# Kernel tuning notes

Measured on AMD Instinct MI355X. Metric: run time of the kernel, lower is better.

The kernel has to match this reference:

```python
import jax, jax.numpy as jnp
import numpy as np

N_NODES = 50000
N_EDGES = 800000
IN_FEATS = 128
OUT_FEATS = 16
NUM_HEADS = 8
NEG_SLOPE = 0.2


def setup_inputs() -> dict:
    key = jax.random.key(0)
    k1, k2, k3, k4, k5 = jax.random.split(key, 5)
    feat = jax.random.normal(k1, (N_NODES, IN_FEATS), dtype=jnp.float32)
    src = jax.random.randint(k2, (N_EDGES,), 0, N_NODES, dtype=jnp.int32)
    dst = jax.random.randint(k3, (N_EDGES,), 0, N_NODES, dtype=jnp.int32)
    # fc weight stored as [in, H*Dout] so y = x @ W (equivalent to torch Linear)
    W = jax.random.normal(k4, (IN_FEATS, NUM_HEADS * OUT_FEATS), dtype=jnp.float32) * 0.05
    attn_weights = jax.random.normal(k5, (2 * NUM_HEADS * OUT_FEATS,), dtype=jnp.float32) * 0.1
    bias = jnp.zeros((NUM_HEADS * OUT_FEATS,), dtype=jnp.float32)
    return {"feat": feat, "W": W, "attn_weights": attn_weights, "bias": bias,
            "src": src, "dst": dst}


def reference(feat, W, attn_weights, bias, src, dst):
    H, D = NUM_HEADS, OUT_FEATS
    N = feat.shape[0]
    # Linear projection: [N, H, D]
    h = (feat @ W).reshape(N, H, D)
    a = attn_weights.reshape(2, H, D)
    # per-node attention logits per head
    e_src = jnp.einsum("nhd,hd->nh", h, a[0])  # source side
    e_dst = jnp.einsum("nhd,hd->nh", h, a[1])  # destination side
    # per-edge scores: [E, H]
    e = e_src[src] + e_dst[dst]
    e = jnp.where(e > 0, e, NEG_SLOPE * e)  # LeakyReLU
    # segment softmax over incoming edges of each dst node
    m = jax.ops.segment_max(e, dst, num_segments=N)          # [N, H]
    m = jnp.where(jnp.isfinite(m), m, 0.0)
    ex = jnp.exp(e - m[dst])                                  # [E, H]
    denom = jax.ops.segment_sum(ex, dst, num_segments=N)     # [N, H]
    alpha = ex / jnp.where(denom[dst] > 0, denom[dst], 1.0)  # [E, H]
    # weighted aggregation of source features: [N, H, D]
    out = jax.ops.segment_sum(alpha[:, :, None] * h[src], dst, num_segments=N)
    out = out + bias.reshape(1, H, D)
    return out
```

## Files before the change

### kernel.cpp

```cpp
#include <hip/hip_runtime.h>
#include <hip/hip_bf16.h>

#define H_HEADS 8
#define D_OUT 16
#define C_FEATS 128
#define NEG_SLOPE 0.2f

typedef __attribute__((ext_vector_type(8))) short short8;
typedef __attribute__((ext_vector_type(4))) float f32x4;

__device__ inline unsigned short f2bf(float f) {
    __hip_bfloat16 b = __float2bfloat16(f);
    return *reinterpret_cast<unsigned short*>(&b);
}
__device__ inline float bf2f(unsigned short u) {
    return __uint_as_float((unsigned)u << 16);
}
__device__ inline float bf_lo(unsigned u) { return __uint_as_float(u << 16); }
__device__ inline float bf_hi(unsigned u) { return __uint_as_float(u & 0xffff0000u); }

__global__ __launch_bounds__(256) void k_prep(const float* __restrict__ W,
                                              unsigned short* __restrict__ Wfh,
                                              unsigned short* __restrict__ Wfl,
                                              int* __restrict__ deg, int N) {
    const int b = blockIdx.x, t = threadIdx.x;
    if (b < 8) {
        const int idx = b * 256 + t;
        const int frag = idx >> 6, lane = idx & 63;
        const int kc = frag >> 3, nt = frag & 7;
        const int kb = kc * 32 + ((lane >> 4) << 3);
        const int col = nt * 16 + (lane & 15);
        unsigned short hs[8], ls[8];
#pragma unroll
        for (int i = 0; i < 8; ++i) {
            const float x = W[(size_t)(kb + i) * C_FEATS + col];
            const unsigned short hh = f2bf(x);
            hs[i] = hh;
            ls[i] = f2bf(x - bf2f(hh));
        }
        uint4 uh, ul;
        uh.x = hs[0] | ((unsigned)hs[1] << 16);
        uh.y = hs[2] | ((unsigned)hs[3] << 16);
        uh.z = hs[4] | ((unsigned)hs[5] << 16);
        uh.w = hs[6] | ((unsigned)hs[7] << 16);
        ul.x = ls[0] | ((unsigned)ls[1] << 16);
        ul.y = ls[2] | ((unsigned)ls[3] << 16);
        ul.z = ls[4] | ((unsigned)ls[5] << 16);
        ul.w = ls[6] | ((unsigned)ls[7] << 16);
        *reinterpret_cast<uint4*>(&Wfh[(size_t)idx * 8]) = uh;
        *reinterpret_cast<uint4*>(&Wfl[(size_t)idx * 8]) = ul;
    } else {
        const int i = (b - 8) * 256 + t;
        if (i < N) deg[i] = 0;
    }
}

__global__ __launch_bounds__(512) void k_gemm_deg(
    const float* __restrict__ feat, const unsigned short* __restrict__ Wfh,
    const unsigned short* __restrict__ Wfl, const int* __restrict__ dst,
    int* __restrict__ deg, int* __restrict__ rank, unsigned short* __restrict__ h16,
    int N, int E, int degBlocks) {
    const int t = threadIdx.x;
    if ((int)blockIdx.x < degBlocks) {
        const int stride = degBlocks * 512;
        for (int e = blockIdx.x * 512 + t; e < E; e += stride)
            rank[e] = atomicAdd(&deg[dst[e]], 1);
        return;
    }
    __shared__ uint4 sW[4096];
    {
        const uint4* gh = reinterpret_cast<const uint4*>(Wfh);
        const uint4* gl = reinterpret_cast<const uint4*>(Wfl);
#pragma unroll
        for (int i = 0; i < 4; ++i) {
            const int j = t + i * 512;
            sW[j] = gh[j];
            sW[j + 2048] = gl[j];
        }
    }
    __syncthreads();

    const int bid = blockIdx.x - degBlocks;
    const int w = t >> 6, lane = t & 63;
    const int rbase = bid * 128 + w * 16;
    const int rowA = rbase + (lane & 15);
    const int ko = (lane >> 4) << 3;
    const bool rv = rowA < N;
    const float* fr = feat + (size_t)rowA * C_FEATS;

    f32x4 acc[8];
#pragma unroll
    for (int nt = 0; nt < 8; ++nt)
#pragma unroll
        for (int j = 0; j < 4; ++j) acc[nt][j] = 0.f;

#pragma unroll
    for (int kc = 0; kc < 4; ++kc) {
        float4 x0 = make_float4(0.f, 0.f, 0.f, 0.f), x1 = x0;
        if (rv) {
            x0 = *reinterpret_cast<const float4*>(fr + kc * 32 + ko);
            x1 = *reinterpret_cast<const float4*>(fr + kc * 32 + ko + 4);
        }
        const float xs[8] = {x0.x, x0.y, x0.z, x0.w, x1.x, x1.y, x1.z, x1.w};
        short8 ah, al;
#pragma unroll
        for (int i = 0; i < 8; ++i) {
            const unsigned short hh = f2bf(xs[i]);
            ah[i] = (short)hh;
            al[i] = (short)f2bf(xs[i] - bf2f(hh));
        }
#pragma unroll
        for (int nt = 0; nt < 8; ++nt) {
            const int fi = (kc * 8 + nt) * 64 + lane;
            const short8 bh = *reinterpret_cast<const short8*>(&sW[fi]);
            const short8 bl = *reinterpret_cast<const short8*>(&sW[fi + 2048]);
            acc[nt] = __builtin_amdgcn_mfma_f32_16x16x32_bf16(ah, bh, acc[nt], 0, 0, 0);
            acc[nt] = __builtin_amdgcn_mfma_f32_16x16x32_bf16(al, bh, acc[nt], 0, 0, 0);
            acc[nt] = __builtin_amdgcn_mfma_f32_16x16x32_bf16(ah, bl, acc[nt], 0, 0, 0);
        }
    }
    const int r0 = rbase + ((lane >> 4) << 2);
    const int colc = lane & 15;
#pragma unroll
    for (int nt = 0; nt < 8; ++nt) {
#pragma unroll
        for (int r = 0; r < 4; ++r) {
            const int row = r0 + r;
            if (row < N)
                h16[(size_t)row * C_FEATS + nt * 16 + colc] = f2bf(acc[nt][r]);
        }
    }
}

__global__ __launch_bounds__(256) void k_logits_bsum(
    const unsigned short* __restrict__ h16, const float* __restrict__ aw,
    float* __restrict__ es, float* __restrict__ ed,
    const int* __restrict__ deg, int* __restrict__ bsum, int N, int LB) {
    const int t = threadIdx.x;
    if ((int)blockIdx.x < LB) {
        const int idx = blockIdx.x * 256 + t;
        if (idx >= N * H_HEADS) return;
        const int n = idx >> 3, hh = idx & 7;
        const uint4 u0 = *reinterpret_cast<const uint4*>(&h16[(size_t)n * C_FEATS + hh * 16]);
        const uint4 u1 = *reinterpret_cast<const uint4*>(&h16[(size_t)n * C_FEATS + hh * 16 + 8]);
        float hv[16];
        hv[0] = bf_lo(u0.x);  hv[1] = bf_hi(u0.x);
        hv[2] = bf_lo(u0.y);  hv[3] = bf_hi(u0.y);
        hv[4] = bf_lo(u0.z);  hv[5] = bf_hi(u0.z);
        hv[6] = bf_lo(u0.w);  hv[7] = bf_hi(u0.w);
        hv[8] = bf_lo(u1.x);  hv[9] = bf_hi(u1.x);
        hv[10] = bf_lo(u1.y); hv[11] = bf_hi(u1.y);
        hv[12] = bf_lo(u1.z); hv[13] = bf_hi(u1.z);
        hv[14] = bf_lo(u1.w); hv[15] = bf_hi(u1.w);
        float s0 = 0.f, s1 = 0.f;
#pragma unroll
        for (int j = 0; j < 16; ++j) {
            s0 = fmaf(hv[j], aw[hh * 16 + j], s0);
            s1 = fmaf(hv[j], aw[C_FEATS + hh * 16 + j], s1);
        }
        es[idx] = s0;
        ed[idx] = s1;
    } else {
        const int i = (blockIdx.x - LB) * 256 + t;
        int v = (i < N) ? deg[i] : 0;
#pragma unroll
        for (int m = 1; m < 64; m <<= 1) v += __shfl_xor(v, m, 64);
        __shared__ int ws[4];
        if ((t & 63) == 0) ws[t >> 6] = v;
        __syncthreads();
        if (t == 0) bsum[blockIdx.x - LB] = ws[0] + ws[1] + ws[2] + ws[3];
    }
}

__device__ inline int block_scan_incl(int v) {
    int lane = threadIdx.x & 63, w = threadIdx.x >> 6;
    int x = v;
#pragma unroll
    for (int d = 1; d < 64; d <<= 1) {
        int u = __shfl_up(x, d, 64);
        if (lane >= d) x += u;
    }
    __shared__ int wsum[4];
    if (lane == 63) wsum[w] = x;
    __syncthreads();
    int add = 0;
    for (int k = 0; k < w; ++k) add += wsum[k];
    return x + add;
}

__global__ void k_scanb(const int* __restrict__ bsum, int* __restrict__ bpre,
                        int NB, int* __restrict__ offs, int N) {
    int t = threadIdx.x;
    int v = (t < NB) ? bsum[t] : 0;
    int incl = block_scan_incl(v);
    if (t < NB) bpre[t] = incl - v;
    if (t == NB - 1) offs[N] = incl;
}

__global__ void k_scanc(const int* __restrict__ deg, const int* __restrict__ bpre,
                        int* __restrict__ offs, int N) {
    int i = blockIdx.x * 256 + threadIdx.x;
    int v = (i < N) ? deg[i] : 0;
    int incl = block_scan_incl(v);
    int excl = incl - v + bpre[blockIdx.x];
    if (i < N) offs[i] = excl;
}

__global__ void k_scatter(const int* __restrict__ src, const int* __restrict__ dst,
                          const int* __restrict__ rank, const int* __restrict__ offs,
                          int* __restrict__ ssorted, int E) {
    int e = blockIdx.x * 256 + threadIdx.x;
    if (e < E)
        ssorted[offs[dst[e]] + rank[e]] = src[e];
}

__global__ __launch_bounds__(256) void k_agg(const unsigned short* __restrict__ h16,
                                             const float* __restrict__ es,
                                             const float* __restrict__ ed,
                                             const int* __restrict__ offs,
                                             const int* __restrict__ ssorted,
                                             const float* __restrict__ bias,
                                             float* __restrict__ out, int N) {
    const int wid = threadIdx.x >> 6, lane = threadIdx.x & 63;
    const int n = blockIdx.x * 4 + wid;
    if (n >= N) return;
    const int beg = offs[n];
    const int deg = offs[n + 1] - beg;

    const int hh = lane >> 3, j0 = lane & 7;
    const float edv = ed[(size_t)n * H_HEADS + hh];

    const int cl = lane & 15, q = lane >> 4;
    const int ah = cl >> 1;
    const int ab = ah << 3;
    float acc[8];
#pragma unroll
    for (int k = 0; k < 8; ++k) acc[k] = 0.f;

    float m = -1e30f, s = 0.f;

    if (deg <= 32) {
        int snc[4];
        float evc[4];
#pragma unroll
        for (int c = 0; c < 4; ++c) {
            const int j = c * 8 + j0;
            const bool va = (j < deg);
            int sn = 0;
            float ev = -1e30f;
            if (va) {
                sn = ssorted[beg + j];
                float t = es[(size_t)sn * H_HEADS + hh] + edv;
                ev = t > 0.f ? t : NEG_SLOPE * t;
                if (ev > m) {
                    s = s * __expf(m - ev) + 1.f;
                    m = ev;
                } else {
                    s += __expf(ev - m);
                }
            }
            snc[c] = sn;
            evc[c] = ev;
        }
#pragma unroll
        for (int msk = 1; msk < 8; msk <<= 1) {
            float mo = __shfl_xor(m, msk, 64);
            float so = __shfl_xor(s, msk, 64);
            float mn = fmaxf(m, mo);
            s = s * __expf(m - mn) + so * __expf(mo - mn);
            m = mn;
        }
        const float inv = (s > 0.f) ? 1.f / s : 0.f;

#pragma unroll
        for (int c = 0; c < 4; ++c) {
            const int cb = c * 8;
            if (cb >= deg) break;
            const float alpha = (cb + j0 < deg) ? __expf(evc[c] - m) * inv : 0.f;
            const int sn = snc[c];
            int rem = deg - cb; if (rem > 8) rem = 8;
#pragma unroll
            for (int e4 = 0; e4 < 2; ++e4) {
                if (4 * e4 >= rem) break;
                const int s0 = __shfl(sn, 4 * e4 + 0, 64);
                const int s1 = __shfl(sn, 4 * e4 + 1, 64);
                const int s2 = __shfl(sn, 4 * e4 + 2, 64);
                const int s3 = __shfl(sn, 4 * e4 + 3, 64);
                const int snq = (q == 0) ? s0 : (q == 1) ? s1 : (q == 2) ? s2 : s3;
                const float al = __shfl(alpha, ab + 4 * e4 + q, 64);
                const uint4 hv = *reinterpret_cast<const uint4*>(
                    &h16[(size_t)snq * C_FEATS + cl * 8]);
                acc[0] = fmaf(al, bf_lo(hv.x), acc[0]);
                acc[1] = fmaf(al, bf_hi(hv.x), acc[1]);
                acc[2] = fmaf(al, bf_lo(hv.y), acc[2]);
                acc[3] = fmaf(al, bf_hi(hv.y), acc[3]);
                acc[4] = fmaf(al, bf_lo(hv.z), acc[4]);
                acc[5] = fmaf(al, bf_hi(hv.z), acc[5]);
                acc[6] = fmaf(al, bf_lo(hv.w), acc[6]);
                acc[7] = fmaf(al, bf_hi(hv.w), acc[7]);
            }
        }
    } else {
        for (int e = j0; e < deg; e += 8) {
            int sn = ssorted[beg + e];
            float ev = es[(size_t)sn * H_HEADS + hh] + edv;
            ev = ev > 0.f ? ev : NEG_SLOPE * ev;
            if (ev > m) {
                s = s * __expf(m - ev) + 1.f;
                m = ev;
            } else {
                s += __expf(ev - m);
            }
        }
#pragma unroll
        for (int msk = 1; msk < 8; msk <<= 1) {
            float mo = __shfl_xor(m, msk, 64);
            float so = __shfl_xor(s, msk, 64);
            float mn = fmaxf(m, mo);
            s = s * __expf(m - mn) + so * __expf(mo - mn);
            m = mn;
        }
        const float inv = (s > 0.f) ? 1.f / s : 0.f;

        for (int cb = 0; cb < deg; cb += 8) {
            const int j = cb + j0;
            int sn = 0;
            float alpha = 0.f;
            if (j < deg) {
                sn = ssorted[beg + j];
                float t = es[(size_t)sn * H_HEADS + hh] + edv;
                t = t > 0.f ? t : NEG_SLOPE * t;
                alpha = __expf(t - m) * inv;
            }
            int rem = deg - cb; if (rem > 8) rem = 8;
#pragma unroll
            for (int e4 = 0; e4 < 2; ++e4) {
                if (4 * e4 >= rem) break;
                const int s0 = __shfl(sn, 4 * e4 + 0, 64);
                const int s1 = __shfl(sn, 4 * e4 + 1, 64);
                const int s2 = __shfl(sn, 4 * e4 + 2, 64);
                const int s3 = __shfl(sn, 4 * e4 + 3, 64);
                const int snq = (q == 0) ? s0 : (q == 1) ? s1 : (q == 2) ? s2 : s3;
                const float al = __shfl(alpha, ab + 4 * e4 + q, 64);
                const uint4 hv = *reinterpret_cast<const uint4*>(
                    &h16[(size_t)snq * C_FEATS + cl * 8]);
                acc[0] = fmaf(al, bf_lo(hv.x), acc[0]);
                acc[1] = fmaf(al, bf_hi(hv.x), acc[1]);
                acc[2] = fmaf(al, bf_lo(hv.y), acc[2]);
                acc[3] = fmaf(al, bf_hi(hv.y), acc[3]);
                acc[4] = fmaf(al, bf_lo(hv.z), acc[4]);
                acc[5] = fmaf(al, bf_hi(hv.z), acc[5]);
                acc[6] = fmaf(al, bf_lo(hv.w), acc[6]);
                acc[7] = fmaf(al, bf_hi(hv.w), acc[7]);
            }
        }
    }

#pragma unroll
    for (int k = 0; k < 8; ++k) {
        acc[k] += __shfl_xor(acc[k], 16, 64);
        acc[k] += __shfl_xor(acc[k], 32, 64);
    }
    if (q == 0) {
        const float4 b0 = *reinterpret_cast<const float4*>(&bias[cl * 8]);
        const float4 b1 = *reinterpret_cast<const float4*>(&bias[cl * 8 + 4]);
        float4 o0 = make_float4(acc[0] + b0.x, acc[1] + b0.y, acc[2] + b0.z, acc[3] + b0.w);
        float4 o1 = make_float4(acc[4] + b1.x, acc[5] + b1.y, acc[6] + b1.z, acc[7] + b1.w);
        *reinterpret_cast<float4*>(&out[(size_t)n * C_FEATS + cl * 8]) = o0;
        *reinterpret_cast<float4*>(&out[(size_t)n * C_FEATS + cl * 8 + 4]) = o1;
    }
}

extern "C" void kernel_launch(void* const* d_in, const int* in_sizes, int n_in,
                              void* d_out, int out_size, void* d_ws, size_t ws_size,
                              hipStream_t stream) {
    const float* feat = (const float*)d_in[0];
    const float* W    = (const float*)d_in[1];
    const float* aw   = (const float*)d_in[2];
    const float* bias = (const float*)d_in[3];
    const int*   src  = (const int*)d_in[4];
    const int*   dst  = (const int*)d_in[5];
    float* out = (float*)d_out;

    const int N = in_sizes[0] / C_FEATS;
    const int E = in_sizes[4];
    const int NB = (N + 255) / 256;
    const int GB = (N + 127) / 128;
    const int DB = 256;
    const int LB = (N * H_HEADS + 255) / 256;

    char* p = (char*)d_ws;
    auto take = [&](size_t bytes) {
        char* q = p;
        p += (bytes + 255) & ~size_t(255);
        return q;
    };
    unsigned short* h16 = (unsigned short*)take((size_t)N * C_FEATS * 2);
    float* es      = (float*)take((size_t)N * H_HEADS * 4);
    float* edt     = (float*)take((size_t)N * H_HEADS * 4);
    int*   deg     = (int*)take((size_t)N * 4);
    int*   offs    = (int*)take((size_t)(N + 1) * 4);
    int*   bsum    = (int*)take((size_t)NB * 4);
    int*   bpre    = (int*)take((size_t)NB * 4);
    int*   ssorted = (int*)take((size_t)E * 4);
    int*   rank    = (int*)take((size_t)E * 4);
    unsigned short* Wfh = (unsigned short*)take((size_t)C_FEATS * C_FEATS * 2);
    unsigned short* Wfl = (unsigned short*)take((size_t)C_FEATS * C_FEATS * 2);
    (void)ws_size;

    k_prep<<<8 + NB, 256, 0, stream>>>(W, Wfh, Wfl, deg, N);
    k_gemm_deg<<<DB + GB, 512, 0, stream>>>(feat, Wfh, Wfl, dst, deg, rank, h16, N, E, DB);
    k_logits_bsum<<<LB + NB, 256, 0, stream>>>(h16, aw, es, edt, deg, bsum, N, LB);
    k_scanb<<<1, 256, 0, stream>>>(bsum, bpre, NB, offs, N);
    k_scanc<<<NB, 256, 0, stream>>>(deg, bpre, offs, N);
    k_scatter<<<(E + 255) / 256, 256, 0, stream>>>(src, dst, rank, offs, ssorted, E);
    k_agg<<<(N + 3) / 4, 256, 0, stream>>>(h16, es, edt, offs, ssorted, bias, out, N);
}
```

Baseline: 119.6 us.

## Fuse attention logits into GEMM epilogue and split degree counting kernel

```diff
diff --git a/kernel.cpp b/kernel.cpp
--- a/kernel.cpp
+++ b/kernel.cpp
@@ -55,18 +55,20 @@
     }
 }
 
-__global__ __launch_bounds__(512) void k_gemm_deg(
+__global__ __launch_bounds__(256) void k_deg_rank(const int* __restrict__ dst,
+                                                  int* __restrict__ deg,
+                                                  int* __restrict__ rank, int E) {
+    const int e = blockIdx.x * 256 + threadIdx.x;
+    if (e < E)
+        rank[e] = atomicAdd(&deg[dst[e]], 1);
+}
+
+__global__ __launch_bounds__(512) void k_gemm(
     const float* __restrict__ feat, const unsigned short* __restrict__ Wfh,
-    const unsigned short* __restrict__ Wfl, const int* __restrict__ dst,
-    int* __restrict__ deg, int* __restrict__ rank, unsigned short* __restrict__ h16,
-    int N, int E, int degBlocks) {
+    const unsigned short* __restrict__ Wfl, const float* __restrict__ aw,
+    unsigned short* __restrict__ h16, float* __restrict__ es,
+    float* __restrict__ ed, int N) {
     const int t = threadIdx.x;
-    if ((int)blockIdx.x < degBlocks) {
-        const int stride = degBlocks * 512;
-        for (int e = blockIdx.x * 512 + t; e < E; e += stride)
-            rank[e] = atomicAdd(&deg[dst[e]], 1);
-        return;
-    }
     __shared__ uint4 sW[4096];
     {
         const uint4* gh = reinterpret_cast<const uint4*>(Wfh);
@@ -80,7 +82,7 @@
     }
     __syncthreads();
 
-    const int bid = blockIdx.x - degBlocks;
+    const int bid = blockIdx.x;
     const int w = t >> 6, lane = t & 63;
     const int rbase = bid * 128 + w * 16;
     const int rowA = rbase + (lane & 15);
@@ -130,46 +132,37 @@
                 h16[(size_t)row * C_FEATS + nt * 16 + colc] = f2bf(acc[nt][r]);
         }
     }
-}
-
-__global__ __launch_bounds__(256) void k_logits_bsum(
-    const unsigned short* __restrict__ h16, const float* __restrict__ aw,
-    float* __restrict__ es, float* __restrict__ ed,
-    const int* __restrict__ deg, int* __restrict__ bsum, int N, int LB) {
-    const int t = threadIdx.x;
-    if ((int)blockIdx.x < LB) {
-        const int idx = blockIdx.x * 256 + t;
-        if (idx >= N * H_HEADS) return;
-        const int n = idx >> 3, hh = idx & 7;
-        const uint4 u0 = *reinterpret_cast<const uint4*>(&h16[(size_t)n * C_FEATS + hh * 16]);
-        const uint4 u1 = *reinterpret_cast<const uint4*>(&h16[(size_t)n * C_FEATS + hh * 16 + 8]);
-        float hv[16];
-        hv[0] = bf_lo(u0.x);  hv[1] = bf_hi(u0.x);
-        hv[2] = bf_lo(u0.y);  hv[3] = bf_hi(u0.y);
-        hv[4] = bf_lo(u0.z);  hv[5] = bf_hi(u0.z);
-        hv[6] = bf_lo(u0.w);  hv[7] = bf_hi(u0.w);
-        hv[8] = bf_lo(u1.x);  hv[9] = bf_hi(u1.x);
-        hv[10] = bf_lo(u1.y); hv[11] = bf_hi(u1.y);
-        hv[12] = bf_lo(u1.z); hv[13] = bf_hi(u1.z);
-        hv[14] = bf_lo(u1.w); hv[15] = bf_hi(u1.w);
-        float s0 = 0.f, s1 = 0.f;
-#pragma unroll
-        for (int j = 0; j < 16; ++j) {
-            s0 = fmaf(hv[j], aw[hh * 16 + j], s0);
-            s1 = fmaf(hv[j], aw[C_FEATS + hh * 16 + j], s1);
-        }
-        es[idx] = s0;
-        ed[idx] = s1;
-    } else {
-        const int i = (blockIdx.x - LB) * 256 + t;
-        int v = (i < N) ? deg[i] : 0;
-#pragma unroll
-        for (int m = 1; m < 64; m <<= 1) v += __shfl_xor(v, m, 64);
-        __shared__ int ws[4];
-        if ((t & 63) == 0) ws[t >> 6] = v;
-        __syncthreads();
-        if (t == 0) bsum[blockIdx.x - LB] = ws[0] + ws[1] + ws[2] + ws[3];
-    }
+#pragma unroll
+    for (int nt = 0; nt < 8; ++nt) {
+        const float wa = aw[nt * 16 + colc];
+        const float wb = aw[C_FEATS + nt * 16 + colc];
+#pragma unroll
+        for (int r = 0; r < 4; ++r) {
+            float pe = acc[nt][r] * wa;
+            float pd = acc[nt][r] * wb;
+#pragma unroll
+            for (int msk = 1; msk <= 8; msk <<= 1) {
+                pe += __shfl_xor(pe, msk, 64);
+                pd += __shfl_xor(pd, msk, 64);
+            }
+            const int row = r0 + r;
+            if (colc == 0 && row < N) {
+                es[(size_t)row * H_HEADS + nt] = pe;
+                ed[(size_t)row * H_HEADS + nt] = pd;
+            }
+        }
+    }
+}
+
+__global__ void k_bsum(const int* __restrict__ deg, int* __restrict__ bsum, int N) {
+    int i = blockIdx.x * 256 + threadIdx.x;
+    int v = (i < N) ? deg[i] : 0;
+#pragma unroll
+    for (int m = 1; m < 64; m <<= 1) v += __shfl_xor(v, m, 64);
+    __shared__ int ws[4];
+    if ((threadIdx.x & 63) == 0) ws[threadIdx.x >> 6] = v;
+    __syncthreads();
+    if (threadIdx.x == 0) bsum[blockIdx.x] = ws[0] + ws[1] + ws[2] + ws[3];
 }
 
 __device__ inline int block_scan_incl(int v) {
@@ -386,8 +379,7 @@
     const int E = in_sizes[4];
     const int NB = (N + 255) / 256;
     const int GB = (N + 127) / 128;
-    const int DB = 256;
-    const int LB = (N * H_HEADS + 255) / 256;
+    const int EB = (E + 255) / 256;
 
     char* p = (char*)d_ws;
     auto take = [&](size_t bytes) {
@@ -409,10 +401,11 @@
     (void)ws_size;
 
     k_prep<<<8 + NB, 256, 0, stream>>>(W, Wfh, Wfl, deg, N);
-    k_gemm_deg<<<DB + GB, 512, 0, stream>>>(feat, Wfh, Wfl, dst, deg, rank, h16, N, E, DB);
-    k_logits_bsum<<<LB + NB, 256, 0, stream>>>(h16, aw, es, edt, deg, bsum, N, LB);
+    k_deg_rank<<<EB, 256, 0, stream>>>(dst, deg, rank, E);
+    k_gemm<<<GB, 512, 0, stream>>>(feat, Wfh, Wfl, aw, h16, es, edt, N);
+    k_bsum<<<NB, 256, 0, stream>>>(deg, bsum, N);
     k_scanb<<<1, 256, 0, stream>>>(bsum, bpre, NB, offs, N);
     k_scanc<<<NB, 256, 0, stream>>>(deg, bpre, offs, N);
-    k_scatter<<<(E + 255) / 256, 256, 0, stream>>>(src, dst, rank, offs, ssorted, E);
+    k_scatter<<<EB, 256, 0, stream>>>(src, dst, rank, offs, ssorted, E);
     k_agg<<<(N + 3) / 4, 256, 0, stream>>>(h16, es, edt, offs, ssorted, bias, out, N);
 }
```

Measured after the change: 133.6 us. +11.8%, slower.
